# Performance work log

Hardware: AMD Instinct MI355X
Metric: run time of the kernel (lower is better)

## Reference

```python
import jax, jax.numpy as jnp
import numpy as np

D_MODEL = 120  # hardcoded in the original module regardless of the d_model arg
C = 10000.0


def setup_inputs() -> dict:
    key = jax.random.key(0)
    kx = jax.random.fold_in(key, 0)
    # (N, L, 4): column 0 unused, columns 1:4 are x/y/z fractional positions
    x = jax.random.uniform(kx, (64, 8192, 4), dtype=jnp.float32)
    D = int(np.ceil(D_MODEL / 6) * 2)  # 40
    div_term = 1.0 / C ** (jnp.arange(0, D, 2, dtype=jnp.float32) / D_MODEL)  # (20,)
    return {"x": x, "div_term": div_term}


def reference(x, div_term):
    # x: (N, L, 4) -> positional encoding (N, L, 120)
    N, L, _ = x.shape
    pos = x[:, :, 1:4]                       # (N, L, 3) x/y/z positions
    sin_inp = pos[..., None] * div_term      # (N, L, 3, 20)
    # interleave sin and cos along the last axis: (N, L, 3, 20, 2) -> (N, L, 3, 40)
    emb = jnp.stack((jnp.sin(sin_inp), jnp.cos(sin_inp)), axis=-1)
    # concat the 3 coordinate embeddings -> (N, L, 120)
    return emb.reshape(N, L, D_MODEL)
```

## Files before the change

### kernel.cpp

```cpp
#include <hip/hip_runtime.h>
#include <hip/hip_bf16.h>


__global__ __launch_bounds__(256) void Embed3D_kernel(
    const float* __restrict__ x,
    const float* __restrict__ div_term,
    float* __restrict__ out,
    int n_quads)
{
    int q = blockIdx.x * blockDim.x + threadIdx.x;
    if (q >= n_quads) return;

    int pos_idx = q / 30;
    int rem     = q - pos_idx * 30;
    int c       = rem / 10;
    int k0      = rem * 2 - c * 20;

    float p  = x[pos_idx * 4 + 1 + c];
    float d0 = div_term[k0];
    float d1 = div_term[k0 + 1];

    float s0, c0, s1, c1;
    __sincosf(p * d0, &s0, &c0);
    __sincosf(p * d1, &s1, &c1);

    float4 v = make_float4(s0, c0, s1, c1);
    reinterpret_cast<float4*>(out)[q] = v;
}

extern "C" void kernel_launch(void* const* d_in, const int* in_sizes, int n_in,
                              void* d_out, int out_size, void* d_ws, size_t ws_size,
                              hipStream_t stream) {
    const float* x        = (const float*)d_in[0];
    const float* div_term = (const float*)d_in[1];
    float* out            = (float*)d_out;

    int n_quads = out_size / 4;
    int block = 256;
    int grid  = (n_quads + block - 1) / block;
    Embed3D_kernel<<<grid, block, 0, stream>>>(x, div_term, out, n_quads);
}
```

Measured before the change: 264.2 us.

## Use 2D blocks, hardware sin/cos builtins, and vectorized position loads

Restructures the launch into 30x32 thread blocks so each thread's coordinate and frequency index come from threadIdx without integer division. It loads positions as float4 and div_term as float2, and replaces __sincosf with the AMDGCN hardware sin/cos builtins on inputs pre-scaled by 1/2π. This is meant to cut ALU and address overhead in a store-heavy kernel. It relies on small argument ranges for the hardware sin/cos accuracy and on the position count being a multiple of 32.

```diff
diff --git a/kernel.cpp b/kernel.cpp
--- a/kernel.cpp
+++ b/kernel.cpp
@@ -2,41 +2,44 @@
 #include <hip/hip_bf16.h>
 
 
-__global__ __launch_bounds__(256) void Embed3D_kernel(
-    const float* __restrict__ x,
-    const float* __restrict__ div_term,
-    float* __restrict__ out,
-    int n_quads)
+constexpr float INV_2PI = 0.15915494309189535f;
+
+__global__ __launch_bounds__(960) void Embed3D_kernel(
+    const float4* __restrict__ x4,
+    const float2* __restrict__ div2,
+    float4* __restrict__ out4)
 {
-    int q = blockIdx.x * blockDim.x + threadIdx.x;
-    if (q >= n_quads) return;
+    const int rem = threadIdx.x;
+    const int pos = blockIdx.x * 32 + threadIdx.y;
 
-    int pos_idx = q / 30;
-    int rem     = q - pos_idx * 30;
-    int c       = rem / 10;
-    int k0      = rem * 2 - c * 20;
+    const int c  = (rem * 205) >> 11;
+    const int kp = rem - 10 * c;
 
-    float p  = x[pos_idx * 4 + 1 + c];
-    float d0 = div_term[k0];
-    float d1 = div_term[k0 + 1];
+    const float4 xv = x4[pos];
+    const float p   = (c == 0) ? xv.y : (c == 1) ? xv.z : xv.w;
 
-    float s0, c0, s1, c1;
-    __sincosf(p * d0, &s0, &c0);
-    __sincosf(p * d1, &s1, &c1);
+    const float2 d = div2[kp];
+    const float r0 = p * d.x * INV_2PI;
+    const float r1 = p * d.y * INV_2PI;
 
-    float4 v = make_float4(s0, c0, s1, c1);
-    reinterpret_cast<float4*>(out)[q] = v;
+    float4 v;
+    v.x = __builtin_amdgcn_sinf(r0);
+    v.y = __builtin_amdgcn_cosf(r0);
+    v.z = __builtin_amdgcn_sinf(r1);
+    v.w = __builtin_amdgcn_cosf(r1);
+
+    out4[pos * 30 + rem] = v;
 }
 
 extern "C" void kernel_launch(void* const* d_in, const int* in_sizes, int n_in,
                               void* d_out, int out_size, void* d_ws, size_t ws_size,
                               hipStream_t stream) {
-    const float* x        = (const float*)d_in[0];
-    const float* div_term = (const float*)d_in[1];
-    float* out            = (float*)d_out;
+    const float4* x4   = (const float4*)d_in[0];
+    const float2* div2 = (const float2*)d_in[1];
+    float4* out4       = (float4*)d_out;
 
-    int n_quads = out_size / 4;
-    int block = 256;
-    int grid  = (n_quads + block - 1) / block;
-    Embed3D_kernel<<<grid, block, 0, stream>>>(x, div_term, out, n_quads);
+    const int positions = in_sizes[0] / 4;
+    dim3 block(30, 32);
+    dim3 grid(positions / 32);
+    Embed3D_kernel<<<grid, block, 0, stream>>>(x4, div2, out4);
 }
```

New measurement: 263.6 us. No clear change (-0.2%).
